# Kernel optimization log

Measured on AMD Instinct MI355X. Metric: run time of the kernel, lower is better.

## Reference

```python
import math
import jax, jax.numpy as jnp
import numpy as np

B, S, H = 8, 1024, 1024
NH = 16
HD = H // NH  # 64


def setup_inputs() -> dict:
    key = jax.random.key(0)
    k1, k2, k3, k4 = jax.random.split(key, 4)
    hidden_states = jax.random.normal(k1, (B, S, H), dtype=jnp.float32)
    attention_mask = jax.random.randint(k2, (B, 1, 1, S), 0, 2, dtype=jnp.int32)
    w_qkv = jax.random.normal(k3, (H, 3 * H), dtype=jnp.float32) * (1.0 / math.sqrt(H))
    b_qkv = jax.random.normal(k4, (3 * H,), dtype=jnp.float32) * 0.02
    return {"hidden_states": hidden_states, "attention_mask": attention_mask,
            "w_qkv": w_qkv, "b_qkv": b_qkv}


def reference(hidden_states, attention_mask, w_qkv, b_qkv):
    b, s, _ = hidden_states.shape
    # fused QKV projection: [b, s, 3H]
    qkv = jnp.einsum('bsh,hk->bsk', hidden_states, w_qkv) + b_qkv
    # view (b, s, nh, 3*hd) -> permute -> chunk last dim (per-head q|k|v layout)
    qkv = qkv.reshape(b, s, NH, 3, HD)
    qkv = jnp.transpose(qkv, (0, 2, 1, 3, 4))      # [b, nh, s, 3, hd]
    q, k, v = qkv[..., 0, :], qkv[..., 1, :], qkv[..., 2, :]
    # raw scores, then FusedScaleMaskSoftmax semantics: scale * scores, mask, fp32 softmax
    scores = jnp.einsum('bhqd,bhkd->bhqk', q, k)
    scale = math.sqrt(HD)  # module passes sqrt(head_dim) as multiplicative scale
    scores = scores.astype(jnp.float32) * scale
    mask = attention_mask != 0                     # nonzero -> masked (padding)
    scores = jnp.where(mask, jnp.float32(-10000.0), scores)
    probs = jax.nn.softmax(scores, axis=-1).astype(hidden_states.dtype)
    # dropout prob = 0 -> identity
    context = jnp.einsum('bhqk,bhkd->bhqd', probs, v)
    context = jnp.transpose(context, (0, 2, 1, 3)).reshape(b, s, NH * HD)
    return context
```

## Files before the change

### kernel.cpp

```cpp
#include <hip/hip_runtime.h>
#include <math.h>

#define Bdim 8
#define Sdim 1024
#define Hdim 1024
#define NHd 16
#define HDd 64
#define N3H 3072

#define Q_OFF   0u
#define K_OFF   16777216u
#define V_OFF   33554432u
#define WH_OFF  41943040u
#define WL_OFF  45088768u
#define AHI_OFF 0u
#define ALO_OFF 8388608u

typedef __bf16 bf16x8 __attribute__((ext_vector_type(8)));
typedef float  f32x4  __attribute__((ext_vector_type(4)));

__device__ __forceinline__ unsigned short f2bf(float x) {
  unsigned b = __builtin_bit_cast(unsigned, x);
  return (unsigned short)((b + 0x7FFFu + ((b >> 16) & 1u)) >> 16);
}
__device__ __forceinline__ float bf2f(unsigned short h) {
  unsigned b = ((unsigned)h) << 16;
  return __builtin_bit_cast(float, b);
}
__device__ __forceinline__ void split_hl(float v, unsigned short& h, unsigned short& l) {
  h = f2bf(v);
  l = f2bf(v - bf2f(h));
}
__device__ __forceinline__ void async16(void* lds, const void* g) {
  __builtin_amdgcn_global_load_lds((const __attribute__((address_space(1))) unsigned int*)g,
                                   (__attribute__((address_space(3))) unsigned int*)lds, 16, 0, 0);
}

__global__ __launch_bounds__(256) void convert_AW(
    const float* __restrict__ A, const float* __restrict__ W,
    unsigned short* __restrict__ aout, unsigned short* __restrict__ ws)
{
  __shared__ float T[64][65];
  const int tid = threadIdx.x;
  int bid = blockIdx.x;
  if (bid < 4096) {
    size_t i = ((size_t)bid * 256 + tid) * 8;
    float4 a0 = *(const float4*)&A[i];
    float4 a1 = *(const float4*)&A[i + 4];
    float av[8] = {a0.x, a0.y, a0.z, a0.w, a1.x, a1.y, a1.z, a1.w};
    unsigned short h[8], l[8];
    #pragma unroll
    for (int j = 0; j < 8; ++j) split_hl(av[j], h[j], l[j]);
    *(uint4*)&aout[AHI_OFF + i] = *(uint4*)h;
    *(uint4*)&aout[ALO_OFF + i] = *(uint4*)l;
    return;
  }
  bid -= 4096;
  const int n0 = (bid % (N3H / 64)) * 64;
  const int k0 = (bid / (N3H / 64)) * 64;
  #pragma unroll
  for (int r = 0; r < 4; ++r) {
    int k = r * 16 + (tid >> 4);
    int n = (tid & 15) * 4;
    float4 v = *(const float4*)&W[(size_t)(k0 + k) * N3H + n0 + n];
    T[k][n + 0] = v.x; T[k][n + 1] = v.y; T[k][n + 2] = v.z; T[k][n + 3] = v.w;
  }
  __syncthreads();
  int n = tid >> 2;
  int kl = (tid & 3) * 16;
  unsigned short h[16], l[16];
  #pragma unroll
  for (int i = 0; i < 16; ++i) split_hl(T[kl + i][n], h[i], l[i]);
  size_t base = (size_t)(n0 + n) * 1024 + k0 + kl;
  *(uint4*)&ws[WH_OFF + base]     = *(uint4*)&h[0];
  *(uint4*)&ws[WH_OFF + base + 8] = *(uint4*)&h[8];
  *(uint4*)&ws[WL_OFF + base]     = *(uint4*)&l[0];
  *(uint4*)&ws[WL_OFF + base + 8] = *(uint4*)&l[8];
}

__global__ __launch_bounds__(512, 2) void qkv_mfma(
    const unsigned short* __restrict__ ao,
    const unsigned short* __restrict__ ws,
    const float* __restrict__ bias,
    unsigned short* __restrict__ wso)
{
  __shared__ __align__(16) unsigned short sA[2][256 * 64];
  __shared__ __align__(16) unsigned short sB[2][192 * 64];

  const int tid  = threadIdx.x;
  const int wave = tid >> 6;
  const int lane = tid & 63;
  const int l16  = lane & 15;
  const int quad = lane >> 4;

  const int bid = blockIdx.x;
  const int xcd = bid & 7;
  const int idx = bid >> 3;
  const int bm = ((xcd >> 1) << 3) | (idx & 7);
  const int bn = ((xcd & 1) << 3) | (((idx >> 5) << 2) | ((idx >> 3) & 3));
  const int n0 = bn * 192;
  const int m0 = bm * 256;

  const int wr = wave >> 2;
  const int wc = wave & 3;
  const int wm = wr * 128;
  const int wn = wc * 48;

  const unsigned short* AH = ao + AHI_OFF;
  const unsigned short* AL = ao + ALO_OFF;
  const unsigned short* WH = ws + WH_OFF;
  const unsigned short* WL = ws + WL_OFF;

  const int rsub  = wave * 8 + (lane >> 3);
  const int colsw = ((lane & 7) ^ (lane >> 3)) * 8;
  const int rdswz = (l16 & 7) << 3;

  f32x4 acc[8][3];
  #pragma unroll
  for (int i = 0; i < 8; ++i)
    #pragma unroll
    for (int j = 0; j < 3; ++j) acc[i][j] = (f32x4){0.f, 0.f, 0.f, 0.f};

  bf16x8 af[4], bf[3];

#define STAGE_A(tt, buf) do { \
    const unsigned short* _ab = ((tt) < 16 || (tt) >= 32) ? AH : AL; \
    const int _ko = ((tt) & 15) * 64; \
    _Pragma("unroll") \
    for (int q = 0; q < 4; ++q) \
      async16(&sA[buf][q * 4096 + wave * 512], \
              &_ab[(size_t)(m0 + q * 64 + rsub) * 1024 + _ko + colsw]); \
  } while (0)

#define STAGE_B(tt, buf) do { \
    const unsigned short* _wb = ((tt) < 32) ? WH : WL; \
    const int _ko = ((tt) & 15) * 64; \
    _Pragma("unroll") \
    for (int q = 0; q < 3; ++q) \
      async16(&sB[buf][q * 4096 + wave * 512], \
              &_wb[(size_t)(n0 + q * 64 + rsub) * 1024 + _ko + colsw]); \
  } while (0)

#define READ_A(h, kk) do { \
    _Pragma("unroll") \
    for (int i = 0; i < 4; ++i) { \
      int row = wm + ((h) * 4 + i) * 16 + l16; \
      af[i] = *(const bf16x8*)&sA[cur][row * 64 + ((((kk) * 32) + quad * 8) ^ rdswz)]; \
    } \
  } while (0)

#define READ_B(kk) do { \
    _Pragma("unroll") \
    for (int j = 0; j < 3; ++j) { \
      int row = wn + j * 16 + l16; \
      bf[j] = *(const bf16x8*)&sB[cur][row * 64 + ((((kk) * 32) + quad * 8) ^ rdswz)]; \
    } \
  } while (0)

#define MFMA12(h) do { \
    __builtin_amdgcn_s_setprio(1); \
    _Pragma("unroll") \
    for (int i = 0; i < 4; ++i) \
      _Pragma("unroll") \
      for (int j = 0; j < 3; ++j) \
        acc[(h) * 4 + i][j] = __builtin_amdgcn_mfma_f32_16x16x32_bf16( \
            af[i], bf[j], acc[(h) * 4 + i][j], 0, 0, 0); \
    __builtin_amdgcn_s_setprio(0); \
  } while (0)

#define BAR    __builtin_amdgcn_s_barrier()
#define SCHEDB __builtin_amdgcn_sched_barrier(0)
#define VMW4   asm volatile("s_waitcnt vmcnt(4)" ::: "memory")
#define VMW0   asm volatile("s_waitcnt vmcnt(0)" ::: "memory")

#define TILE_BODY(P, t_) do { \
    const int cur = (P); \
     \
    READ_A(0, 0); READ_B(0); \
    if ((t_) + 1 < 48) STAGE_B((t_) + 1, 1 - (P)); \
    BAR; SCHEDB; MFMA12(0); BAR; \
     \
    READ_A(1, 0); \
    BAR; SCHEDB; MFMA12(1); BAR; \
     \
    READ_A(0, 1); READ_B(1); \
    BAR; SCHEDB; MFMA12(0); BAR; \
     \
    READ_A(1, 1); \
    BAR; SCHEDB; MFMA12(1); BAR; \
     \
    if ((t_) + 2 < 48) STAGE_A((t_) + 2, (P)); \
    if ((t_) + 1 < 48) { \
      if ((t_) + 2 < 48) { VMW4; } else { VMW0; } \
      BAR; \
    } \
  } while (0)

  STAGE_A(0, 0); STAGE_B(0, 0);
  STAGE_A(1, 1);
  VMW4;
  BAR;

  for (int t = 0; t < 48; t += 2) {
    TILE_BODY(0, t);
    TILE_BODY(1, t + 1);
  }

  const int bb   = m0 >> 10;
  const int bh   = bb * NHd + bn;
  const int srow = (m0 & 1023) + wm;

  #pragma unroll
  for (int j = 0; j < 3; ++j) {
    const int colb  = wn + j * 16;
    const int which = colb >> 6;
    const int d0    = colb & 63;
    const float bsj = bias[n0 + colb + l16];

    if (which == 0) {
      unsigned short* dst = wso + Q_OFF + ((size_t)bh * Sdim) * 128;
      #pragma unroll
      for (int i = 0; i < 8; ++i)
        #pragma unroll
        for (int r = 0; r < 4; ++r) {
          int s = srow + i * 16 + quad * 4 + r;
          unsigned short h, l;
          split_hl(acc[i][j][r] + bsj, h, l);
          dst[(size_t)s * 128 + d0 + l16]      = h;
          dst[(size_t)s * 128 + 64 + d0 + l16] = l;
        }
    } else if (which == 1) {
      const int c = d0 + l16;
      #pragma unroll
      for (int i = 0; i < 8; ++i) {
        int tile = (srow + i * 16) >> 6;
        int spb  = (i * 16 + quad * 4) & 63;
        unsigned short* dst = wso + K_OFF + (size_t)bh * 131072 + (size_t)tile * 8192;
        #pragma unroll
        for (int r = 0; r < 4; ++r) {
          int sp = spb + r;
          int idx = ((((sp >> 4) * 4 + (c >> 5)) * 64 + ((c >> 3) & 3) * 16 + (sp & 15)) << 3) + (c & 7);
          unsigned short h, l;
          split_hl(acc[i][j][r] + bsj, h, l);
          dst[idx]        = h;
          dst[idx + 1024] = l;
        }
      }
    } else {
      const int dr = d0 + l16;
      #pragma unroll
      for (int i = 0; i < 8; ++i) {
        int tile = (srow + i * 16) >> 6;
        int ky   = (i * 16 + quad * 4) & 63;
        unsigned short* dst = wso + V_OFF + (size_t)bh * 65536 + (size_t)tile * 4096;
        int idx = ((((dr >> 4) * 2 + (ky >> 5)) * 64 + ((ky >> 3) & 3) * 16 + (dr & 15)) << 3) + (ky & 7);
        unsigned short p[4];
        #pragma unroll
        for (int r = 0; r < 4; ++r) p[r] = f2bf(acc[i][j][r] + bsj);
        *(uint2*)&dst[idx] = *(uint2*)p;
      }
    }
  }

#undef STAGE_A
#undef STAGE_B
#undef READ_A
#undef READ_B
#undef MFMA12
#undef BAR
#undef SCHEDB
#undef VMW4
#undef VMW0
#undef TILE_BODY
}

__global__ __launch_bounds__(256, 4) void attn_mfma(
    const unsigned short* __restrict__ qhl,
    const unsigned short* __restrict__ khl,
    const unsigned short* __restrict__ vt,
    const int* __restrict__ mask,
    float* __restrict__ out)
{
  __shared__ unsigned short Ks[8192];
  __shared__ unsigned short Vs[4096];
  __shared__ unsigned short Pw[4][1024];
  __shared__ float msks[1024];

  const int tid  = threadIdx.x;
  const int wave = tid >> 6;
  const int lane = tid & 63;
  const int l16  = lane & 15;
  const int quad = lane >> 4;

  const int bh = blockIdx.x & 127;
  const int qt = blockIdx.x >> 7;
  const int bb = bh >> 4;
  const int q0 = qt * 64;

  const unsigned short* kplane = khl + (size_t)bh * 131072;
  const unsigned short* vplane = vt  + (size_t)bh * 65536;

  {
    int4 mv = *(const int4*)&mask[bb * Sdim + tid * 4];
    msks[tid * 4 + 0] = mv.x ? 1.f : 0.f;
    msks[tid * 4 + 1] = mv.y ? 1.f : 0.f;
    msks[tid * 4 + 2] = mv.z ? 1.f : 0.f;
    msks[tid * 4 + 3] = mv.w ? 1.f : 0.f;
  }

  bf16x8 qf[4];
  {
    int row = q0 + wave * 16 + l16;
    const unsigned short* src = qhl + ((size_t)bh * Sdim + row) * 128;
    #pragma unroll
    for (int kk = 0; kk < 4; ++kk)
      qf[kk] = *(const bf16x8*)&src[kk * 32 + quad * 8];
  }

  f32x4 O[4] = {{0.f,0.f,0.f,0.f},{0.f,0.f,0.f,0.f},{0.f,0.f,0.f,0.f},{0.f,0.f,0.f,0.f}};
  float mrow[4] = {-INFINITY, -INFINITY, -INFINITY, -INFINITY};
  float lrow[4] = {0.f, 0.f, 0.f, 0.f};

  #pragma unroll 1
  for (int kt = 0; kt < 16; ++kt) {
    __syncthreads();
    {
      const unsigned short* ksrc = kplane + (size_t)kt * 8192;
      const unsigned short* vsrc = vplane + (size_t)kt * 4096;
      #pragma unroll
      for (int r = 0; r < 4; ++r)
        async16(&Ks[(r * 256 + tid) * 8], &ksrc[(size_t)(r * 256 + tid) * 8]);
      #pragma unroll
      for (int r = 0; r < 2; ++r)
        async16(&Vs[(r * 256 + tid) * 8], &vsrc[(size_t)(r * 256 + tid) * 8]);
    }
    __syncthreads();

    f32x4 sc[4];
    #pragma unroll
    for (int ns = 0; ns < 4; ++ns) {
      f32x4 c = {0.f, 0.f, 0.f, 0.f};
      bf16x8 kf0 = *(const bf16x8*)&Ks[((ns * 4 + 0) * 64 + lane) * 8];
      bf16x8 kf1 = *(const bf16x8*)&Ks[((ns * 4 + 1) * 64 + lane) * 8];
      bf16x8 kf2 = *(const bf16x8*)&Ks[((ns * 4 + 2) * 64 + lane) * 8];
      bf16x8 kf3 = *(const bf16x8*)&Ks[((ns * 4 + 3) * 64 + lane) * 8];
      c = __builtin_amdgcn_mfma_f32_16x16x32_bf16(qf[0], kf0, c, 0, 0, 0);
      c = __builtin_amdgcn_mfma_f32_16x16x32_bf16(qf[1], kf1, c, 0, 0, 0);
      c = __builtin_amdgcn_mfma_f32_16x16x32_bf16(qf[2], kf0, c, 0, 0, 0);
      c = __builtin_amdgcn_mfma_f32_16x16x32_bf16(qf[3], kf1, c, 0, 0, 0);
      c = __builtin_amdgcn_mfma_f32_16x16x32_bf16(qf[0], kf2, c, 0, 0, 0);
      c = __builtin_amdgcn_mfma_f32_16x16x32_bf16(qf[1], kf3, c, 0, 0, 0);
      sc[ns] = c;
    }

    float rmax[4] = {-INFINITY, -INFINITY, -INFINITY, -INFINITY};
    #pragma unroll
    for (int ns = 0; ns < 4; ++ns) {
      float mk = msks[kt * 64 + ns * 16 + l16];
      #pragma unroll
      for (int r = 0; r < 4; ++r) {
        float s = (mk != 0.f) ? -10000.f : sc[ns][r] * 8.f;
        sc[ns][r] = s;
        rmax[r] = fmaxf(rmax[r], s);
      }
    }
    #pragma unroll
    for (int r = 0; r < 4; ++r) {
      float v = rmax[r];
      v = fmaxf(v, __shfl_xor(v, 1, 16));
      v = fmaxf(v, __shfl_xor(v, 2, 16));
      v = fmaxf(v, __shfl_xor(v, 4, 16));
      v = fmaxf(v, __shfl_xor(v, 8, 16));
      rmax[r] = v;
    }

    float alpha[4];
    #pragma unroll
    for (int r = 0; r < 4; ++r) {
      float mn = fmaxf(mrow[r], rmax[r]);
      alpha[r] = __expf(mrow[r] - mn);
      mrow[r] = mn;
      lrow[r] *= alpha[r];
    }
    #pragma unroll
    for (int d = 0; d < 4; ++d)
      #pragma unroll
      for (int r = 0; r < 4; ++r) O[d][r] *= alpha[r];

    float rsum[4] = {0.f, 0.f, 0.f, 0.f};
    #pragma unroll
    for (int ns = 0; ns < 4; ++ns) {
      int key = ns * 16 + l16;
      int cbase = (((key >> 5) * 4 + ((key >> 3) & 3)) * 16 + quad * 4) * 8 + (key & 7);
      #pragma unroll
      for (int r = 0; r < 4; ++r) {
        float p = __expf(sc[ns][r] - mrow[r]);
        rsum[r] += p;
        Pw[wave][cbase + r * 8] = f2bf(p);
      }
    }
    #pragma unroll
    for (int r = 0; r < 4; ++r) {
      float v = rsum[r];
      v += __shfl_xor(v, 1, 16);
      v += __shfl_xor(v, 2, 16);
      v += __shfl_xor(v, 4, 16);
      v += __shfl_xor(v, 8, 16);
      lrow[r] += v;
    }

    bf16x8 pf[2];
    #pragma unroll
    for (int kk = 0; kk < 2; ++kk)
      pf[kk] = *(const bf16x8*)&Pw[wave][((kk * 4 + quad) * 16 + l16) * 8];
    #pragma unroll
    for (int d = 0; d < 4; ++d)
      #pragma unroll
      for (int kk = 0; kk < 2; ++kk) {
        bf16x8 vf = *(const bf16x8*)&Vs[((d * 2 + kk) * 64 + lane) * 8];
        O[d] = __builtin_amdgcn_mfma_f32_16x16x32_bf16(pf[kk], vf, O[d], 0, 0, 0);
      }
  }

  const int h = bh & 15;
  #pragma unroll
  for (int r = 0; r < 4; ++r) {
    float inv = 1.f / lrow[r];
    int q = q0 + wave * 16 + quad * 4 + r;
    float* dst = out + ((size_t)bb * Sdim + q) * Hdim + h * HDd;
    #pragma unroll
    for (int d = 0; d < 4; ++d)
      dst[d * 16 + l16] = O[d][r] * inv;
  }
}

extern "C" void kernel_launch(void* const* d_in, const int* in_sizes, int n_in,
                              void* d_out, int out_size, void* d_ws, size_t ws_size,
                              hipStream_t stream) {
  const float* hs   = (const float*)d_in[0];
  const int*   mask = (const int*)d_in[1];
  const float* w    = (const float*)d_in[2];
  const float* bias = (const float*)d_in[3];
  float* out = (float*)d_out;
  unsigned short* ws = (unsigned short*)d_ws;
  unsigned short* ao = (unsigned short*)d_out;

  convert_AW<<<4096 + (N3H / 64) * (1024 / 64), 256, 0, stream>>>(hs, w, ao, ws);

  qkv_mfma<<<dim3(512), 512, 0, stream>>>(ao, ws, bias, ws);

  attn_mfma<<<Bdim * NHd * (Sdim / 64), 256, 0, stream>>>(
      ws + Q_OFF, ws + K_OFF, ws + V_OFF, mask, out);
}
```

Measured before the change: 376.7 us.

## Widen QKV GEMM tile to 256x384 and switch to 32x32x16 MFMA

The QKV projection kernel's block tile grows from 256x192 to 256x384, so each block covers two full heads, and the grid drops from 512 to 256 blocks. The inner product switches from 16x16x32 MFMA to 32x32x16 MFMA, with one combined A/B fragment read per k-substep, which cuts LDS fragment traffic per FLOP and raises operand reuse. The B staging is split into two halves spread across the k-steps, and the epilogue is rewritten for the 32x32 accumulator layout. In exchange, the accumulators double to 192 floats per thread, which may spill under the unchanged launch bounds of (512, 2). LDS use rises to 160 KB, so only one block fits per CU, and 256 blocks give a single wave with less latency hiding.

```diff
diff --git a/kernel.cpp b/kernel.cpp
--- a/kernel.cpp
+++ b/kernel.cpp
@@ -18,6 +18,7 @@
 
 typedef __bf16 bf16x8 __attribute__((ext_vector_type(8)));
 typedef float  f32x4  __attribute__((ext_vector_type(4)));
+typedef float  f32x16 __attribute__((ext_vector_type(16)));
 
 __device__ __forceinline__ unsigned short f2bf(float x) {
   unsigned b = __builtin_bit_cast(unsigned, x);
@@ -85,26 +86,24 @@
     unsigned short* __restrict__ wso)
 {
   __shared__ __align__(16) unsigned short sA[2][256 * 64];
-  __shared__ __align__(16) unsigned short sB[2][192 * 64];
+  __shared__ __align__(16) unsigned short sB[2][384 * 64];
 
   const int tid  = threadIdx.x;
   const int wave = tid >> 6;
   const int lane = tid & 63;
-  const int l16  = lane & 15;
-  const int quad = lane >> 4;
+  const int l32  = lane & 31;
+  const int hi   = lane >> 5;
 
   const int bid = blockIdx.x;
   const int xcd = bid & 7;
-  const int idx = bid >> 3;
-  const int bm = ((xcd >> 1) << 3) | (idx & 7);
-  const int bn = ((xcd & 1) << 3) | (((idx >> 5) << 2) | ((idx >> 3) & 3));
-  const int n0 = bn * 192;
-  const int m0 = bm * 256;
-
-  const int wr = wave >> 2;
-  const int wc = wave & 3;
-  const int wm = wr * 128;
-  const int wn = wc * 48;
+  const int g   = bid >> 3;
+  const int bm  = ((xcd >> 1) << 3) | (g & 7);
+  const int bn  = ((xcd & 1) << 2) | (g >> 3);
+  const int m0  = bm * 256;
+  const int n0  = bn * 384;
+
+  const int wm = (wave >> 2) * 128;
+  const int wn = (wave & 3) * 96;
 
   const unsigned short* AH = ao + AHI_OFF;
   const unsigned short* AL = ao + ALO_OFF;
@@ -113,13 +112,14 @@
 
   const int rsub  = wave * 8 + (lane >> 3);
   const int colsw = ((lane & 7) ^ (lane >> 3)) * 8;
-  const int rdswz = (l16 & 7) << 3;
-
-  f32x4 acc[8][3];
+  const int rdswz = (lane & 7) << 3;
+
+  f32x16 acc[4][3];
   #pragma unroll
-  for (int i = 0; i < 8; ++i)
-    #pragma unroll
-    for (int j = 0; j < 3; ++j) acc[i][j] = (f32x4){0.f, 0.f, 0.f, 0.f};
+  for (int i = 0; i < 4; ++i)
+    #pragma unroll
+    for (int j = 0; j < 3; ++j)
+      acc[i][j] = (f32x16){0.f,0.f,0.f,0.f,0.f,0.f,0.f,0.f,0.f,0.f,0.f,0.f,0.f,0.f,0.f,0.f};
 
   bf16x8 af[4], bf[3];
 
@@ -132,39 +132,33 @@
               &_ab[(size_t)(m0 + q * 64 + rsub) * 1024 + _ko + colsw]); \
   } while (0)
 
-#define STAGE_B(tt, buf) do { \
+#define STAGE_B_H(tt, buf, h_) do { \
     const unsigned short* _wb = ((tt) < 32) ? WH : WL; \
     const int _ko = ((tt) & 15) * 64; \
     _Pragma("unroll") \
-    for (int q = 0; q < 3; ++q) \
+    for (int q = (h_) * 3; q < (h_) * 3 + 3; ++q) \
       async16(&sB[buf][q * 4096 + wave * 512], \
               &_wb[(size_t)(n0 + q * 64 + rsub) * 1024 + _ko + colsw]); \
   } while (0)
 
-#define READ_A(h, kk) do { \
+#define READ_AB(s) do { \
+    const int _c = (((s) * 16 + hi * 8) ^ rdswz); \
     _Pragma("unroll") \
-    for (int i = 0; i < 4; ++i) { \
-      int row = wm + ((h) * 4 + i) * 16 + l16; \
-      af[i] = *(const bf16x8*)&sA[cur][row * 64 + ((((kk) * 32) + quad * 8) ^ rdswz)]; \
-    } \
+    for (int i = 0; i < 4; ++i) \
+      af[i] = *(const bf16x8*)&sA[cur][(wm + i * 32 + l32) * 64 + _c]; \
+    _Pragma("unroll") \
+    for (int j = 0; j < 3; ++j) \
+      bf[j] = *(const bf16x8*)&sB[cur][(wn + j * 32 + l32) * 64 + _c]; \
   } while (0)
 
-#define READ_B(kk) do { \
-    _Pragma("unroll") \
-    for (int j = 0; j < 3; ++j) { \
-      int row = wn + j * 16 + l16; \
-      bf[j] = *(const bf16x8*)&sB[cur][row * 64 + ((((kk) * 32) + quad * 8) ^ rdswz)]; \
-    } \
-  } while (0)
-
-#define MFMA12(h) do { \
+#define MFMA12 do { \
     __builtin_amdgcn_s_setprio(1); \
     _Pragma("unroll") \
     for (int i = 0; i < 4; ++i) \
       _Pragma("unroll") \
       for (int j = 0; j < 3; ++j) \
-        acc[(h) * 4 + i][j] = __builtin_amdgcn_mfma_f32_16x16x32_bf16( \
-            af[i], bf[j], acc[(h) * 4 + i][j], 0, 0, 0); \
+        acc[i][j] = __builtin_amdgcn_mfma_f32_32x32x16_bf16( \
+            af[i], bf[j], acc[i][j], 0, 0, 0); \
     __builtin_amdgcn_s_setprio(0); \
   } while (0)
 
@@ -175,19 +169,16 @@
 
 #define TILE_BODY(P, t_) do { \
     const int cur = (P); \
-     \
-    READ_A(0, 0); READ_B(0); \
-    if ((t_) + 1 < 48) STAGE_B((t_) + 1, 1 - (P)); \
-    BAR; SCHEDB; MFMA12(0); BAR; \
-     \
-    READ_A(1, 0); \
-    BAR; SCHEDB; MFMA12(1); BAR; \
-     \
-    READ_A(0, 1); READ_B(1); \
-    BAR; SCHEDB; MFMA12(0); BAR; \
-     \
-    READ_A(1, 1); \
-    BAR; SCHEDB; MFMA12(1); BAR; \
+    READ_AB(0); \
+    if ((t_) + 1 < 48) STAGE_B_H((t_) + 1, 1 - (P), 0); \
+    BAR; SCHEDB; MFMA12; BAR; \
+    READ_AB(1); \
+    if ((t_) + 1 < 48) STAGE_B_H((t_) + 1, 1 - (P), 1); \
+    BAR; SCHEDB; MFMA12; BAR; \
+    READ_AB(2); \
+    BAR; SCHEDB; MFMA12; BAR; \
+    READ_AB(3); \
+    BAR; SCHEDB; MFMA12; BAR; \
      \
     if ((t_) + 2 < 48) STAGE_A((t_) + 2, (P)); \
     if ((t_) + 1 < 48) { \
@@ -196,7 +187,7 @@
     } \
   } while (0)
 
-  STAGE_A(0, 0); STAGE_B(0, 0);
+  STAGE_A(0, 0); STAGE_B_H(0, 0, 0); STAGE_B_H(0, 0, 1);
   STAGE_A(1, 1);
   VMW4;
   BAR;
@@ -207,65 +198,66 @@
   }
 
   const int bb   = m0 >> 10;
-  const int bh   = bb * NHd + bn;
   const int srow = (m0 & 1023) + wm;
 
   #pragma unroll
   for (int j = 0; j < 3; ++j) {
-    const int colb  = wn + j * 16;
-    const int which = colb >> 6;
-    const int d0    = colb & 63;
-    const float bsj = bias[n0 + colb + l16];
-
-    if (which == 0) {
-      unsigned short* dst = wso + Q_OFF + ((size_t)bh * Sdim) * 128;
-      #pragma unroll
-      for (int i = 0; i < 8; ++i)
+    const int colb   = wn + j * 32;
+    const int head   = (bn << 1) + (colb >= 192 ? 1 : 0);
+    const int within = (colb >= 192) ? colb - 192 : colb;
+    const int which  = within >> 6;
+    const int dsub   = within & 63;
+    const int bh     = bb * NHd + head;
+    const float bsj  = bias[n0 + colb + l32];
+
+    #pragma unroll
+    for (int i = 0; i < 4; ++i) {
+      const int sbase = srow + i * 32;
+      const int tile  = sbase >> 6;
+      const int kbase = sbase & 32;
+
+      if (which == 0) {
+        unsigned short* dst = wso + Q_OFF + ((size_t)bh * Sdim + sbase) * 128;
+        const int d = dsub + l32;
         #pragma unroll
-        for (int r = 0; r < 4; ++r) {
-          int s = srow + i * 16 + quad * 4 + r;
-          unsigned short h, l;
-          split_hl(acc[i][j][r] + bsj, h, l);
-          dst[(size_t)s * 128 + d0 + l16]      = h;
-          dst[(size_t)s * 128 + 64 + d0 + l16] = l;
+        for (int r = 0; r < 16; ++r) {
+          int rl = (r & 3) + 8 * (r >> 2) + 4 * hi;
+          unsigned short h_, l_;
+          split_hl(acc[i][j][r] + bsj, h_, l_);
+          dst[(size_t)rl * 128 + d]      = h_;
+          dst[(size_t)rl * 128 + 64 + d] = l_;
         }
-    } else if (which == 1) {
-      const int c = d0 + l16;
-      #pragma unroll
-      for (int i = 0; i < 8; ++i) {
-        int tile = (srow + i * 16) >> 6;
-        int spb  = (i * 16 + quad * 4) & 63;
+      } else if (which == 1) {
+        const int c = dsub + l32;
         unsigned short* dst = wso + K_OFF + (size_t)bh * 131072 + (size_t)tile * 8192;
         #pragma unroll
-        for (int r = 0; r < 4; ++r) {
-          int sp = spb + r;
+        for (int r = 0; r < 16; ++r) {
+          int sp = kbase + (r & 3) + 8 * (r >> 2) + 4 * hi;
           int idx = ((((sp >> 4) * 4 + (c >> 5)) * 64 + ((c >> 3) & 3) * 16 + (sp & 15)) << 3) + (c & 7);
-          unsigned short h, l;
-          split_hl(acc[i][j][r] + bsj, h, l);
-          dst[idx]        = h;
-          dst[idx + 1024] = l;
+          unsigned short h_, l_;
+          split_hl(acc[i][j][r] + bsj, h_, l_);
+          dst[idx]        = h_;
+          dst[idx + 1024] = l_;
+        }
+      } else {
+        const int dr = dsub + l32;
+        unsigned short* dst = wso + V_OFF + (size_t)bh * 65536 + (size_t)tile * 4096;
+        #pragma unroll
+        for (int rg = 0; rg < 4; ++rg) {
+          int ky0 = kbase + rg * 8 + 4 * hi;
+          int idx = ((((dr >> 4) * 2 + (ky0 >> 5)) * 64 + ((ky0 >> 3) & 3) * 16 + (dr & 15)) << 3) + (ky0 & 7);
+          unsigned short p[4];
+          #pragma unroll
+          for (int e = 0; e < 4; ++e) p[e] = f2bf(acc[i][j][rg * 4 + e] + bsj);
+          *(uint2*)&dst[idx] = *(uint2*)p;
         }
       }
-    } else {
-      const int dr = d0 + l16;
-      #pragma unroll
-      for (int i = 0; i < 8; ++i) {
-        int tile = (srow + i * 16) >> 6;
-        int ky   = (i * 16 + quad * 4) & 63;
-        unsigned short* dst = wso + V_OFF + (size_t)bh * 65536 + (size_t)tile * 4096;
-        int idx = ((((dr >> 4) * 2 + (ky >> 5)) * 64 + ((ky >> 3) & 3) * 16 + (dr & 15)) << 3) + (ky & 7);
-        unsigned short p[4];
-        #pragma unroll
-        for (int r = 0; r < 4; ++r) p[r] = f2bf(acc[i][j][r] + bsj);
-        *(uint2*)&dst[idx] = *(uint2*)p;
-      }
     }
   }
 
 #undef STAGE_A
-#undef STAGE_B
-#undef READ_A
-#undef READ_B
+#undef STAGE_B_H
+#undef READ_AB
 #undef MFMA12
 #undef BAR
 #undef SCHEDB
@@ -447,7 +439,7 @@
 
   convert_AW<<<4096 + (N3H / 64) * (1024 / 64), 256, 0, stream>>>(hs, w, ao, ws);
 
-  qkv_mfma<<<dim3(512), 512, 0, stream>>>(ao, ws, bias, ws);
+  qkv_mfma<<<dim3(256), 512, 0, stream>>>(ao, ws, bias, ws);
 
   attn_mfma<<<Bdim * NHd * (Sdim / 64), 256, 0, stream>>>(
       ws + Q_OFF, ws + K_OFF, ws + V_OFF, mask, out);
```

Result: no change. 375.7 us (-0.2%).
